# Kernel optimization log

Hardware: AMD Instinct MI355X
Metric: run time of the kernel (lower is better)

Reference implementation:

```python
import jax, jax.numpy as jnp
import numpy as np

E, H, I, T, K = 32, 1024, 768, 2048, 8


def setup_inputs() -> dict:
    key = jax.random.key(0)
    ks = jax.random.split(key, 6)
    hidden_states = jax.random.normal(ks[0], (T, H), dtype=jnp.float32)
    routing_weights = jax.random.uniform(ks[1], (T, K), dtype=jnp.float32)
    selected_experts = jax.random.randint(ks[2], (T, K), 0, E, dtype=jnp.int32)
    scale = 0.02
    gate_proj = jax.random.normal(ks[3], (E, I, H), dtype=jnp.float32) * scale
    up_proj = jax.random.normal(ks[4], (E, I, H), dtype=jnp.float32) * scale
    down_proj = jax.random.normal(ks[5], (E, H, I), dtype=jnp.float32) * scale
    return {
        "hidden_states": hidden_states,
        "routing_weights": routing_weights,
        "selected_experts": selected_experts,
        "gate_proj": gate_proj,
        "up_proj": up_proj,
        "down_proj": down_proj,
    }


def reference(hidden_states, routing_weights, selected_experts, gate_proj, up_proj, down_proj):
    # hidden_states: [T, H]; routing_weights/selected_experts: [T, K]
    # gate/up: [E, I, H]; down: [E, H, I]
    T_, _ = hidden_states.shape
    E_ = gate_proj.shape[0]
    # combine[t, e] = sum_k routing_weights[t, k] * 1[selected_experts[t, k] == e]
    combine = jnp.zeros((T_, E_), hidden_states.dtype).at[
        jnp.arange(T_)[:, None], selected_experts
    ].add(routing_weights)
    g = jnp.einsum('th,eih->eti', hidden_states, gate_proj)   # [E, T, I]
    u = jnp.einsum('th,eih->eti', hidden_states, up_proj)     # [E, T, I]
    h = jax.nn.silu(g) * u                                    # SwiGLU
    d = jnp.einsum('eti,ehi->eth', h, down_proj)              # [E, T, H]
    out = jnp.einsum('eth,te->th', d, combine)                # weighted combine
    return out
```

## Files before the change

kernel.cpp:

```cpp
#include <hip/hip_runtime.h>
#include <hip/hip_bf16.h>
#include <math.h>

#define E_N 32
#define H_N 1024
#define I_N 768
#define T_N 2048
#define K_N 8
#define MT  128
#define NPAIRS (T_N * K_N)
#define MAX_SLOTS (NPAIRS + E_N * MT)
#define MAX_TILES (NPAIRS / MT + E_N)

typedef __attribute__((ext_vector_type(8))) short bf16x8;
typedef __attribute__((ext_vector_type(4))) short bf16x4;
typedef __attribute__((ext_vector_type(8))) float f32x8;
typedef __attribute__((ext_vector_type(4))) float f32x4;

__device__ __forceinline__ unsigned pk2(float a, float b) {
    unsigned ua = __float_as_uint(a) + 0x8000u;
    unsigned ub = __float_as_uint(b) + 0x8000u;
    return (ua >> 16) | (ub & 0xffff0000u);
}
__device__ __forceinline__ bf16x8 cvt8(f32x8 v) {
    union { unsigned u[4]; bf16x8 h; } r;
    r.u[0] = pk2(v[0], v[1]); r.u[1] = pk2(v[2], v[3]);
    r.u[2] = pk2(v[4], v[5]); r.u[3] = pk2(v[6], v[7]);
    return r.h;
}
__device__ __forceinline__ float bf2f(short s) {
    return __uint_as_float(((unsigned)(unsigned short)s) << 16);
}

__device__ __forceinline__ void gload16(const void* g, void* l) {
    __builtin_amdgcn_global_load_lds(
        (const __attribute__((address_space(1))) unsigned int*)g,
        (__attribute__((address_space(3))) unsigned int*)l, 16, 0, 0);
}

__global__ __launch_bounds__(256) void hist_kernel(const int* __restrict__ sel,
                                                   int* __restrict__ cnt_g) {
    __shared__ int cnt[E_N];
    int tid = threadIdx.x;
    if (tid < E_N) cnt[tid] = 0;
    __syncthreads();
    int p = blockIdx.x * 256 + tid;
    atomicAdd(&cnt[sel[p]], 1);
    __syncthreads();
    if (tid < E_N) atomicAdd(&cnt_g[tid], cnt[tid]);
}

__global__ void scan_kernel(const int* __restrict__ cnt_g,
                            int* __restrict__ off_g,
                            int* __restrict__ tile_expert,
                            int* __restrict__ tile_row0,
                            int* __restrict__ n_tiles_out) {
    if (threadIdx.x == 0) {
        int acc = 0, tt = 0;
        for (int e = 0; e < E_N; ++e) {
            off_g[e] = acc;
            int nt = (cnt_g[e] + MT - 1) / MT;
            for (int i = 0; i < nt; ++i) {
                tile_expert[tt] = e;
                tile_row0[tt] = acc + i * MT;
                ++tt;
            }
            acc += nt * MT;
        }
        *n_tiles_out = tt;
    }
}

__global__ __launch_bounds__(256) void place_kernel(
    const int* __restrict__ sel,
    const int* __restrict__ off_g,
    int* __restrict__ cur_g,
    int* __restrict__ slot_token,
    int* __restrict__ pair_slot) {
    int p = blockIdx.x * 256 + threadIdx.x;
    int e = sel[p];
    int slot = off_g[e] + atomicAdd(&cur_g[e], 1);
    slot_token[slot] = p / K_N;
    pair_slot[p] = slot;
}

__global__ __launch_bounds__(256) void gather_kernel(
    const float* __restrict__ hs,
    const int* __restrict__ slot_token,
    short* __restrict__ x_buf) {
    int idx = blockIdx.x * 256 + threadIdx.x;
    int slot = idx >> 8;
    int pos = (idx & 255) * 4;
    int tok = slot_token[slot];
    union { unsigned u[2]; bf16x4 s; } o;
    if (tok >= 0) {
        f32x4 v = *(const f32x4*)(hs + (size_t)tok * H_N + pos);
        o.u[0] = pk2(v[0], v[1]);
        o.u[1] = pk2(v[2], v[3]);
    } else {
        o.u[0] = 0; o.u[1] = 0;
    }
    *(bf16x4*)(x_buf + (size_t)slot * H_N + pos) = o.s;
}

__global__ __launch_bounds__(256) void cvt2_kernel(
    const float* __restrict__ s0, short* __restrict__ d0,
    const float* __restrict__ s1, short* __restrict__ d1, int n8) {
    int i = blockIdx.x * 256 + threadIdx.x;
    int stride = gridDim.x * 256;
    for (; i < n8; i += stride) {
        f32x8 v0 = *(const f32x8*)(s0 + (size_t)i * 8);
        *(bf16x8*)(d0 + (size_t)i * 8) = cvt8(v0);
        f32x8 v1 = *(const f32x8*)(s1 + (size_t)i * 8);
        *(bf16x8*)(d1 + (size_t)i * 8) = cvt8(v1);
    }
}
__global__ __launch_bounds__(256) void cvt_kernel(
    const float* __restrict__ src, short* __restrict__ dst, int n8) {
    int i = blockIdx.x * 256 + threadIdx.x;
    int stride = gridDim.x * 256;
    for (; i < n8; i += stride) {
        f32x8 v = *(const f32x8*)(src + (size_t)i * 8);
        *(bf16x8*)(dst + (size_t)i * 8) = cvt8(v);
    }
}

__global__ __launch_bounds__(256, 2) void gateup_kernel(
    const short* __restrict__ x_buf,
    const short* __restrict__ wg,
    const short* __restrict__ wu,
    const int* __restrict__ tile_expert,
    const int* __restrict__ tile_row0,
    const int* __restrict__ n_tiles,
    __hip_bfloat16* __restrict__ h_buf) {
    int id = blockIdx.x;
    int W = (id & 7) * 120 + (id >> 3);
    int tile = W % MAX_TILES;
    int ycol = W / MAX_TILES;
    if (tile >= *n_tiles) return;
    __shared__ short sA[2][128 * 32];
    __shared__ short sG[2][128 * 32];
    __shared__ short sU[2][128 * 32];
    int e = tile_expert[tile];
    int row0 = tile_row0[tile];
    int col0 = ycol * 128;
    int tid = threadIdx.x;
    int wave = tid >> 6, lane = tid & 63, quad = lane >> 4, r16 = lane & 15;
    int m0w = (wave >> 1) * 64, n0w = (wave & 1) * 64;
    int srow = lane >> 2;
    int scb = (lane & 3) * 8;

    f32x4 accG[4][4], accU[4][4];
#pragma unroll
    for (int i = 0; i < 4; ++i)
#pragma unroll
        for (int j = 0; j < 4; ++j) {
            accG[i][j] = (f32x4){0.f, 0.f, 0.f, 0.f};
            accU[i][j] = (f32x4){0.f, 0.f, 0.f, 0.f};
        }

    const short* Ag = x_buf + (size_t)row0 * H_N;
    const short* Gg = wg + ((size_t)e * I_N + col0) * H_N;
    const short* Ug = wu + ((size_t)e * I_N + col0) * H_N;

#pragma unroll 1
    for (int k0 = 0; k0 < H_N; k0 += 64) {
        __syncthreads();
#pragma unroll
        for (int c = 0; c < 2; ++c) {
            int rb = (wave * 2 + c) * 16;
            size_t goff = (size_t)(rb + srow) * H_N + k0 + scb;
            gload16(Ag + goff,      &sA[0][rb * 32]);
            gload16(Ag + goff + 32, &sA[1][rb * 32]);
            gload16(Gg + goff,      &sG[0][rb * 32]);
            gload16(Gg + goff + 32, &sG[1][rb * 32]);
            gload16(Ug + goff,      &sU[0][rb * 32]);
            gload16(Ug + goff + 32, &sU[1][rb * 32]);
        }
        __syncthreads();
#pragma unroll
        for (int ks = 0; ks < 2; ++ks) {
            bf16x8 af[4], bg[4], bu[4];
#pragma unroll
            for (int mi = 0; mi < 4; ++mi)
                af[mi] = *(const bf16x8*)&sA[ks][(m0w + mi * 16 + r16) * 32 + quad * 8];
#pragma unroll
            for (int ni = 0; ni < 4; ++ni) {
                bg[ni] = *(const bf16x8*)&sG[ks][(n0w + ni * 16 + r16) * 32 + quad * 8];
                bu[ni] = *(const bf16x8*)&sU[ks][(n0w + ni * 16 + r16) * 32 + quad * 8];
            }
            __builtin_amdgcn_s_setprio(1);
#pragma unroll
            for (int mi = 0; mi < 4; ++mi)
#pragma unroll
                for (int ni = 0; ni < 4; ++ni) {
                    accG[mi][ni] = __builtin_amdgcn_mfma_f32_16x16x32_bf16(af[mi], bg[ni], accG[mi][ni], 0, 0, 0);
                    accU[mi][ni] = __builtin_amdgcn_mfma_f32_16x16x32_bf16(af[mi], bu[ni], accU[mi][ni], 0, 0, 0);
                }
            __builtin_amdgcn_s_setprio(0);
        }
    }
#pragma unroll
    for (int mi = 0; mi < 4; ++mi)
#pragma unroll
        for (int ni = 0; ni < 4; ++ni)
#pragma unroll
            for (int r = 0; r < 4; ++r) {
                int m = m0w + mi * 16 + quad * 4 + r;
                int n = col0 + n0w + ni * 16 + r16;
                float g = accG[mi][ni][r], u = accU[mi][ni][r];
                float hval = g * u / (1.0f + __expf(-g));
                h_buf[(size_t)(row0 + m) * I_N + n] = __float2bfloat16(hval);
            }
}

__global__ __launch_bounds__(256, 3) void down_kernel(
    const __hip_bfloat16* __restrict__ h_buf,
    const short* __restrict__ wd,
    const int* __restrict__ tile_expert,
    const int* __restrict__ tile_row0,
    const int* __restrict__ n_tiles,
    short* __restrict__ d_buf) {
    int id = blockIdx.x;
    int W = (id & 7) * 160 + (id >> 3);
    int tile = W % MAX_TILES;
    int ycol = W / MAX_TILES;
    if (tile >= *n_tiles) return;
    __shared__ short sA[2][128 * 32];
    __shared__ short sB[2][128 * 32];
    int e = tile_expert[tile];
    int row0 = tile_row0[tile];
    int col0 = ycol * 128;
    int tid = threadIdx.x;
    int wave = tid >> 6, lane = tid & 63, quad = lane >> 4, r16 = lane & 15;
    int m0w = (wave >> 1) * 64, n0w = (wave & 1) * 64;
    int srow = lane >> 2;
    int scb = (lane & 3) * 8;

    f32x4 acc[4][4];
#pragma unroll
    for (int i = 0; i < 4; ++i)
#pragma unroll
        for (int j = 0; j < 4; ++j) acc[i][j] = (f32x4){0.f, 0.f, 0.f, 0.f};

    const short* Ag = (const short*)h_buf + (size_t)row0 * I_N;
    const short* Bg = wd + ((size_t)e * H_N + col0) * I_N;

#pragma unroll 1
    for (int k0 = 0; k0 < I_N; k0 += 64) {
        __syncthreads();
#pragma unroll
        for (int c = 0; c < 2; ++c) {
            int rb = (wave * 2 + c) * 16;
            size_t goff = (size_t)(rb + srow) * I_N + k0 + scb;
            gload16(Ag + goff,      &sA[0][rb * 32]);
            gload16(Ag + goff + 32, &sA[1][rb * 32]);
            gload16(Bg + goff,      &sB[0][rb * 32]);
            gload16(Bg + goff + 32, &sB[1][rb * 32]);
        }
        __syncthreads();
#pragma unroll
        for (int ks = 0; ks < 2; ++ks) {
            bf16x8 af[4], bf[4];
#pragma unroll
            for (int mi = 0; mi < 4; ++mi)
                af[mi] = *(const bf16x8*)&sA[ks][(m0w + mi * 16 + r16) * 32 + quad * 8];
#pragma unroll
            for (int ni = 0; ni < 4; ++ni)
                bf[ni] = *(const bf16x8*)&sB[ks][(n0w + ni * 16 + r16) * 32 + quad * 8];
            __builtin_amdgcn_s_setprio(1);
#pragma unroll
            for (int mi = 0; mi < 4; ++mi)
#pragma unroll
                for (int ni = 0; ni < 4; ++ni)
                    acc[mi][ni] = __builtin_amdgcn_mfma_f32_16x16x32_bf16(af[mi], bf[ni], acc[mi][ni], 0, 0, 0);
            __builtin_amdgcn_s_setprio(0);
        }
    }
#pragma unroll
    for (int mi = 0; mi < 4; ++mi)
#pragma unroll
        for (int ni = 0; ni < 4; ++ni)
#pragma unroll
            for (int r = 0; r < 4; ++r) {
                int m = m0w + mi * 16 + quad * 4 + r;
                int n = col0 + n0w + ni * 16 + r16;
                unsigned u = __float_as_uint(acc[mi][ni][r]) + 0x8000u;
                d_buf[(size_t)(row0 + m) * H_N + n] = (short)(u >> 16);
            }
}

__global__ __launch_bounds__(256) void combine_kernel(
    const short* __restrict__ d_buf,
    const int* __restrict__ pair_slot,
    const float* __restrict__ rw,
    float* __restrict__ out) {
    int idx = blockIdx.x * blockDim.x + threadIdx.x;
    int t = idx >> 10;
    int h = idx & (H_N - 1);
    float acc = 0.f;
#pragma unroll
    for (int k = 0; k < K_N; ++k) {
        int slot = pair_slot[t * K_N + k];
        float w = rw[t * K_N + k];
        acc += w * bf2f(d_buf[(size_t)slot * H_N + h]);
    }
    out[idx] = acc;
}

extern "C" void kernel_launch(void* const* d_in, const int* in_sizes, int n_in,
                              void* d_out, int out_size, void* d_ws, size_t ws_size,
                              hipStream_t stream) {
    const float* hs   = (const float*)d_in[0];
    const float* rw   = (const float*)d_in[1];
    const int*   sel  = (const int*)d_in[2];
    const float* gate = (const float*)d_in[3];
    const float* up   = (const float*)d_in[4];
    const float* down = (const float*)d_in[5];
    float* out = (float*)d_out;

    const size_t WN = (size_t)E_N * I_N * H_N;
    char* ws = (char*)d_ws;
    int* slot_token  = (int*)ws;  ws += ((size_t)MAX_SLOTS * 4 + 255) / 256 * 256;
    int* pair_slot   = (int*)ws;  ws += ((size_t)NPAIRS * 4 + 255) / 256 * 256;
    int* tile_expert = (int*)ws;  ws += ((size_t)MAX_TILES * 4 + 255) / 256 * 256;
    int* tile_row0   = (int*)ws;  ws += ((size_t)MAX_TILES * 4 + 255) / 256 * 256;
    int* n_tiles     = (int*)ws;  ws += 256;
    int* cnt_g       = (int*)ws;  ws += 256;
    int* cur_g       = (int*)ws;  ws += 256;
    int* off_g       = (int*)ws;  ws += 256;
    short* x_buf = (short*)ws;    ws += ((size_t)MAX_SLOTS * H_N * 2 + 255) / 256 * 256;
    __hip_bfloat16* h_buf = (__hip_bfloat16*)ws;
    ws += ((size_t)MAX_SLOTS * I_N * 2 + 255) / 256 * 256;
    short* wg = (short*)ws;
    short* wu = wg + WN;
    short* wd = wg;
    short* d_buf = x_buf;

    hipMemsetAsync(slot_token, 0xFF, (size_t)MAX_SLOTS * 4, stream);
    hipMemsetAsync(cnt_g, 0, 512, stream);

    hist_kernel<<<NPAIRS / 256, 256, 0, stream>>>(sel, cnt_g);
    scan_kernel<<<1, 64, 0, stream>>>(cnt_g, off_g, tile_expert, tile_row0, n_tiles);
    place_kernel<<<NPAIRS / 256, 256, 0, stream>>>(sel, off_g, cur_g,
                                                   slot_token, pair_slot);
    gather_kernel<<<(MAX_SLOTS * H_N / 4) / 256, 256, 0, stream>>>(hs, slot_token, x_buf);

    const int N8 = (int)(WN / 8);
    cvt2_kernel<<<2048, 256, 0, stream>>>(gate, wg, up, wu, N8);

    gateup_kernel<<<MAX_TILES * (I_N / 128), 256, 0, stream>>>(
        x_buf, wg, wu, tile_expert, tile_row0, n_tiles, h_buf);

    cvt_kernel<<<2048, 256, 0, stream>>>(down, wd, N8);

    down_kernel<<<MAX_TILES * (H_N / 128), 256, 0, stream>>>(
        h_buf, wd, tile_expert, tile_row0, n_tiles, d_buf);

    combine_kernel<<<(T_N * H_N) / 256, 256, 0, stream>>>(d_buf, pair_slot,
                                                          rw, out);
}
```

Before: 513.0 us.

## Fuse fp32-to-bf16 weight conversion into gate/up and down GEMM kernels

Drops the separate weight conversion kernels. The GEMMs now read fp32 expert weights directly, convert them to bf16 in registers and store them to swizzled shared memory. Activation tiles are double-buffered with a register prefetch of the next K-slice, and the K-step is halved to 32. This removes a full write and re-read of bf16 weight copies, but each tile now re-reads fp32 weights (twice the bytes) once per token tile, and there are more barriers per K.

```diff
diff --git a/kernel.cpp b/kernel.cpp
--- a/kernel.cpp
+++ b/kernel.cpp
@@ -103,32 +103,10 @@
     *(bf16x4*)(x_buf + (size_t)slot * H_N + pos) = o.s;
 }
 
-__global__ __launch_bounds__(256) void cvt2_kernel(
-    const float* __restrict__ s0, short* __restrict__ d0,
-    const float* __restrict__ s1, short* __restrict__ d1, int n8) {
-    int i = blockIdx.x * 256 + threadIdx.x;
-    int stride = gridDim.x * 256;
-    for (; i < n8; i += stride) {
-        f32x8 v0 = *(const f32x8*)(s0 + (size_t)i * 8);
-        *(bf16x8*)(d0 + (size_t)i * 8) = cvt8(v0);
-        f32x8 v1 = *(const f32x8*)(s1 + (size_t)i * 8);
-        *(bf16x8*)(d1 + (size_t)i * 8) = cvt8(v1);
-    }
-}
-__global__ __launch_bounds__(256) void cvt_kernel(
-    const float* __restrict__ src, short* __restrict__ dst, int n8) {
-    int i = blockIdx.x * 256 + threadIdx.x;
-    int stride = gridDim.x * 256;
-    for (; i < n8; i += stride) {
-        f32x8 v = *(const f32x8*)(src + (size_t)i * 8);
-        *(bf16x8*)(dst + (size_t)i * 8) = cvt8(v);
-    }
-}
-
 __global__ __launch_bounds__(256, 2) void gateup_kernel(
     const short* __restrict__ x_buf,
-    const short* __restrict__ wg,
-    const short* __restrict__ wu,
+    const float* __restrict__ gate,
+    const float* __restrict__ up,
     const int* __restrict__ tile_expert,
     const int* __restrict__ tile_row0,
     const int* __restrict__ n_tiles,
@@ -139,16 +117,20 @@
     int ycol = W / MAX_TILES;
     if (tile >= *n_tiles) return;
     __shared__ short sA[2][128 * 32];
-    __shared__ short sG[2][128 * 32];
-    __shared__ short sU[2][128 * 32];
+    __shared__ short sG[128 * 32];
+    __shared__ short sU[128 * 32];
     int e = tile_expert[tile];
     int row0 = tile_row0[tile];
     int col0 = ycol * 128;
     int tid = threadIdx.x;
     int wave = tid >> 6, lane = tid & 63, quad = lane >> 4, r16 = lane & 15;
     int m0w = (wave >> 1) * 64, n0w = (wave & 1) * 64;
-    int srow = lane >> 2;
-    int scb = (lane & 3) * 8;
+    int srow_d = lane >> 2;
+    int scb_sw = (((lane & 3) ^ (srow_d & 3)) * 8);
+    int srow_r = tid >> 2;
+    int scol = (tid & 3) * 8;
+    int wchk = ((tid & 3) ^ (srow_r & 3)) * 8;
+    int qsw = (quad ^ (r16 & 3)) * 8;
 
     f32x4 accG[4][4], accU[4][4];
 #pragma unroll
@@ -160,45 +142,67 @@
         }
 
     const short* Ag = x_buf + (size_t)row0 * H_N;
-    const short* Gg = wg + ((size_t)e * I_N + col0) * H_N;
-    const short* Ug = wu + ((size_t)e * I_N + col0) * H_N;
-
+    const float* Gg = gate + ((size_t)e * I_N + col0) * H_N;
+    const float* Ug = up + ((size_t)e * I_N + col0) * H_N;
+
+    f32x8 pg[2], pu[2];
+#pragma unroll
+    for (int r = 0; r < 2; ++r) {
+        int row = r * 64 + srow_r;
+        pg[r] = *(const f32x8*)(Gg + (size_t)row * H_N + scol);
+        pu[r] = *(const f32x8*)(Ug + (size_t)row * H_N + scol);
+    }
+#pragma unroll
+    for (int c = 0; c < 2; ++c) {
+        int rb = (wave * 2 + c) * 16;
+        gload16(Ag + (size_t)(rb + srow_d) * H_N + scb_sw, &sA[0][rb * 32]);
+    }
+
+    int cur = 0;
 #pragma unroll 1
-    for (int k0 = 0; k0 < H_N; k0 += 64) {
+    for (int k0 = 0; k0 < H_N; k0 += 32) {
         __syncthreads();
 #pragma unroll
-        for (int c = 0; c < 2; ++c) {
-            int rb = (wave * 2 + c) * 16;
-            size_t goff = (size_t)(rb + srow) * H_N + k0 + scb;
-            gload16(Ag + goff,      &sA[0][rb * 32]);
-            gload16(Ag + goff + 32, &sA[1][rb * 32]);
-            gload16(Gg + goff,      &sG[0][rb * 32]);
-            gload16(Gg + goff + 32, &sG[1][rb * 32]);
-            gload16(Ug + goff,      &sU[0][rb * 32]);
-            gload16(Ug + goff + 32, &sU[1][rb * 32]);
+        for (int r = 0; r < 2; ++r) {
+            int row = r * 64 + srow_r;
+            *(bf16x8*)&sG[row * 32 + wchk] = cvt8(pg[r]);
+            *(bf16x8*)&sU[row * 32 + wchk] = cvt8(pu[r]);
         }
         __syncthreads();
-#pragma unroll
-        for (int ks = 0; ks < 2; ++ks) {
-            bf16x8 af[4], bg[4], bu[4];
-#pragma unroll
-            for (int mi = 0; mi < 4; ++mi)
-                af[mi] = *(const bf16x8*)&sA[ks][(m0w + mi * 16 + r16) * 32 + quad * 8];
+        if (k0 + 32 < H_N) {
+            int kn = k0 + 32;
+#pragma unroll
+            for (int r = 0; r < 2; ++r) {
+                int row = r * 64 + srow_r;
+                pg[r] = *(const f32x8*)(Gg + (size_t)row * H_N + kn + scol);
+                pu[r] = *(const f32x8*)(Ug + (size_t)row * H_N + kn + scol);
+            }
+#pragma unroll
+            for (int c = 0; c < 2; ++c) {
+                int rb = (wave * 2 + c) * 16;
+                gload16(Ag + (size_t)(rb + srow_d) * H_N + kn + scb_sw,
+                        &sA[cur ^ 1][rb * 32]);
+            }
+        }
+        bf16x8 af[4], bg[4], bu[4];
+#pragma unroll
+        for (int mi = 0; mi < 4; ++mi)
+            af[mi] = *(const bf16x8*)&sA[cur][(m0w + mi * 16 + r16) * 32 + qsw];
+#pragma unroll
+        for (int ni = 0; ni < 4; ++ni) {
+            bg[ni] = *(const bf16x8*)&sG[(n0w + ni * 16 + r16) * 32 + qsw];
+            bu[ni] = *(const bf16x8*)&sU[(n0w + ni * 16 + r16) * 32 + qsw];
+        }
+        __builtin_amdgcn_s_setprio(1);
+#pragma unroll
+        for (int mi = 0; mi < 4; ++mi)
 #pragma unroll
             for (int ni = 0; ni < 4; ++ni) {
-                bg[ni] = *(const bf16x8*)&sG[ks][(n0w + ni * 16 + r16) * 32 + quad * 8];
-                bu[ni] = *(const bf16x8*)&sU[ks][(n0w + ni * 16 + r16) * 32 + quad * 8];
-            }
-            __builtin_amdgcn_s_setprio(1);
-#pragma unroll
-            for (int mi = 0; mi < 4; ++mi)
-#pragma unroll
-                for (int ni = 0; ni < 4; ++ni) {
-                    accG[mi][ni] = __builtin_amdgcn_mfma_f32_16x16x32_bf16(af[mi], bg[ni], accG[mi][ni], 0, 0, 0);
-                    accU[mi][ni] = __builtin_amdgcn_mfma_f32_16x16x32_bf16(af[mi], bu[ni], accU[mi][ni], 0, 0, 0);
-                }
-            __builtin_amdgcn_s_setprio(0);
-        }
+                accG[mi][ni] = __builtin_amdgcn_mfma_f32_16x16x32_bf16(af[mi], bg[ni], accG[mi][ni], 0, 0, 0);
+                accU[mi][ni] = __builtin_amdgcn_mfma_f32_16x16x32_bf16(af[mi], bu[ni], accU[mi][ni], 0, 0, 0);
+            }
+        __builtin_amdgcn_s_setprio(0);
+        cur ^= 1;
     }
 #pragma unroll
     for (int mi = 0; mi < 4; ++mi)
@@ -216,7 +220,7 @@
 
 __global__ __launch_bounds__(256, 3) void down_kernel(
     const __hip_bfloat16* __restrict__ h_buf,
-    const short* __restrict__ wd,
+    const float* __restrict__ down,
     const int* __restrict__ tile_expert,
     const int* __restrict__ tile_row0,
     const int* __restrict__ n_tiles,
@@ -227,15 +231,19 @@
     int ycol = W / MAX_TILES;
     if (tile >= *n_tiles) return;
     __shared__ short sA[2][128 * 32];
-    __shared__ short sB[2][128 * 32];
+    __shared__ short sB[128 * 32];
     int e = tile_expert[tile];
     int row0 = tile_row0[tile];
     int col0 = ycol * 128;
     int tid = threadIdx.x;
     int wave = tid >> 6, lane = tid & 63, quad = lane >> 4, r16 = lane & 15;
     int m0w = (wave >> 1) * 64, n0w = (wave & 1) * 64;
-    int srow = lane >> 2;
-    int scb = (lane & 3) * 8;
+    int srow_d = lane >> 2;
+    int scb_sw = (((lane & 3) ^ (srow_d & 3)) * 8);
+    int srow_r = tid >> 2;
+    int scol = (tid & 3) * 8;
+    int wchk = ((tid & 3) ^ (srow_r & 3)) * 8;
+    int qsw = (quad ^ (r16 & 3)) * 8;
 
     f32x4 acc[4][4];
 #pragma unroll
@@ -244,38 +252,59 @@
         for (int j = 0; j < 4; ++j) acc[i][j] = (f32x4){0.f, 0.f, 0.f, 0.f};
 
     const short* Ag = (const short*)h_buf + (size_t)row0 * I_N;
-    const short* Bg = wd + ((size_t)e * H_N + col0) * I_N;
-
+    const float* Bg = down + ((size_t)e * H_N + col0) * I_N;
+
+    f32x8 pb[2];
+#pragma unroll
+    for (int r = 0; r < 2; ++r) {
+        int row = r * 64 + srow_r;
+        pb[r] = *(const f32x8*)(Bg + (size_t)row * I_N + scol);
+    }
+#pragma unroll
+    for (int c = 0; c < 2; ++c) {
+        int rb = (wave * 2 + c) * 16;
+        gload16(Ag + (size_t)(rb + srow_d) * I_N + scb_sw, &sA[0][rb * 32]);
+    }
+
+    int cur = 0;
 #pragma unroll 1
-    for (int k0 = 0; k0 < I_N; k0 += 64) {
+    for (int k0 = 0; k0 < I_N; k0 += 32) {
         __syncthreads();
 #pragma unroll
-        for (int c = 0; c < 2; ++c) {
-            int rb = (wave * 2 + c) * 16;
-            size_t goff = (size_t)(rb + srow) * I_N + k0 + scb;
-            gload16(Ag + goff,      &sA[0][rb * 32]);
-            gload16(Ag + goff + 32, &sA[1][rb * 32]);
-            gload16(Bg + goff,      &sB[0][rb * 32]);
-            gload16(Bg + goff + 32, &sB[1][rb * 32]);
+        for (int r = 0; r < 2; ++r) {
+            int row = r * 64 + srow_r;
+            *(bf16x8*)&sB[row * 32 + wchk] = cvt8(pb[r]);
         }
         __syncthreads();
-#pragma unroll
-        for (int ks = 0; ks < 2; ++ks) {
-            bf16x8 af[4], bf[4];
-#pragma unroll
-            for (int mi = 0; mi < 4; ++mi)
-                af[mi] = *(const bf16x8*)&sA[ks][(m0w + mi * 16 + r16) * 32 + quad * 8];
+        if (k0 + 32 < I_N) {
+            int kn = k0 + 32;
+#pragma unroll
+            for (int r = 0; r < 2; ++r) {
+                int row = r * 64 + srow_r;
+                pb[r] = *(const f32x8*)(Bg + (size_t)row * I_N + kn + scol);
+            }
+#pragma unroll
+            for (int c = 0; c < 2; ++c) {
+                int rb = (wave * 2 + c) * 16;
+                gload16(Ag + (size_t)(rb + srow_d) * I_N + kn + scb_sw,
+                        &sA[cur ^ 1][rb * 32]);
+            }
+        }
+        bf16x8 af[4], bf[4];
+#pragma unroll
+        for (int mi = 0; mi < 4; ++mi)
+            af[mi] = *(const bf16x8*)&sA[cur][(m0w + mi * 16 + r16) * 32 + qsw];
+#pragma unroll
+        for (int ni = 0; ni < 4; ++ni)
+            bf[ni] = *(const bf16x8*)&sB[(n0w + ni * 16 + r16) * 32 + qsw];
+        __builtin_amdgcn_s_setprio(1);
+#pragma unroll
+        for (int mi = 0; mi < 4; ++mi)
 #pragma unroll
             for (int ni = 0; ni < 4; ++ni)
-                bf[ni] = *(const bf16x8*)&sB[ks][(n0w + ni * 16 + r16) * 32 + quad * 8];
-            __builtin_amdgcn_s_setprio(1);
-#pragma unroll
-            for (int mi = 0; mi < 4; ++mi)
-#pragma unroll
-                for (int ni = 0; ni < 4; ++ni)
-                    acc[mi][ni] = __builtin_amdgcn_mfma_f32_16x16x32_bf16(af[mi], bf[ni], acc[mi][ni], 0, 0, 0);
-            __builtin_amdgcn_s_setprio(0);
-        }
+                acc[mi][ni] = __builtin_amdgcn_mfma_f32_16x16x32_bf16(af[mi], bf[ni], acc[mi][ni], 0, 0, 0);
+        __builtin_amdgcn_s_setprio(0);
+        cur ^= 1;
     }
 #pragma unroll
     for (int mi = 0; mi < 4; ++mi)
@@ -319,7 +348,6 @@
     const float* down = (const float*)d_in[5];
     float* out = (float*)d_out;
 
-    const size_t WN = (size_t)E_N * I_N * H_N;
     char* ws = (char*)d_ws;
     int* slot_token  = (int*)ws;  ws += ((size_t)MAX_SLOTS * 4 + 255) / 256 * 256;
     int* pair_slot   = (int*)ws;  ws += ((size_t)NPAIRS * 4 + 255) / 256 * 256;
@@ -331,10 +359,6 @@
     int* off_g       = (int*)ws;  ws += 256;
     short* x_buf = (short*)ws;    ws += ((size_t)MAX_SLOTS * H_N * 2 + 255) / 256 * 256;
     __hip_bfloat16* h_buf = (__hip_bfloat16*)ws;
-    ws += ((size_t)MAX_SLOTS * I_N * 2 + 255) / 256 * 256;
-    short* wg = (short*)ws;
-    short* wu = wg + WN;
-    short* wd = wg;
     short* d_buf = x_buf;
 
     hipMemsetAsync(slot_token, 0xFF, (size_t)MAX_SLOTS * 4, stream);
@@ -346,16 +370,11 @@
                                                    slot_token, pair_slot);
     gather_kernel<<<(MAX_SLOTS * H_N / 4) / 256, 256, 0, stream>>>(hs, slot_token, x_buf);
 
-    const int N8 = (int)(WN / 8);
-    cvt2_kernel<<<2048, 256, 0, stream>>>(gate, wg, up, wu, N8);
-
     gateup_kernel<<<MAX_TILES * (I_N / 128), 256, 0, stream>>>(
-        x_buf, wg, wu, tile_expert, tile_row0, n_tiles, h_buf);
-
-    cvt_kernel<<<2048, 256, 0, stream>>>(down, wd, N8);
+        x_buf, gate, up, tile_expert, tile_row0, n_tiles, h_buf);
 
     down_kernel<<<MAX_TILES * (H_N / 128), 256, 0, stream>>>(
-        h_buf, wd, tile_expert, tile_row0, n_tiles, d_buf);
+        h_buf, down, tile_expert, tile_row0, n_tiles, d_buf);
 
     combine_kernel<<<(T_N * H_N) / 256, 256, 0, stream>>>(d_buf, pair_slot,
                                                           rw, out);
```

New measurement: 500.5 us. 2.4% less time.
